# Performance work log

Hardware: AMD Instinct MI355X
Metric: run time of the kernel (lower is better)

Reference implementation:

```python
import jax, jax.numpy as jnp
import numpy as np

N = 100_000      # nodes
E = 1_600_000    # edges (before self-loops)
IN, OUT, HID = 64, 32, 64
BN_EPS = 1e-5

def _mlp(h, w1, b1, g, beta, w2, b2):
    # PyG MLP (num_layers=2, plain_last=True): Linear -> BatchNorm(train) -> ReLU -> Linear
    h = h @ w1 + b1
    mu = jnp.mean(h, axis=0)
    var = jnp.var(h, axis=0)
    h = (h - mu) * jax.lax.rsqrt(var + BN_EPS) * g + beta
    return jax.nn.relu(h) @ w2 + b2

def setup_inputs() -> dict:
    key = jax.random.key(0)
    ks = jax.random.split(key, 12)
    def rn(k, shape):
        fan_in = shape[0]
        return jax.random.normal(k, shape, jnp.float32) / np.sqrt(fan_in)
    x = jax.random.normal(ks[0], (N, IN), jnp.float32)
    pos = jax.random.normal(ks[1], (N, 3), jnp.float32)
    edge_index = jax.random.randint(ks[2], (2, E), 0, N, jnp.int64)
    return {
        "x": x, "pos": pos, "edge_index": edge_index,
        "w_lin": rn(ks[3], (IN, OUT)), "w_src": rn(ks[4], (IN, OUT)), "w_dst": rn(ks[5], (IN, OUT)),
        "pos_w1": rn(ks[6], (3, HID)), "pos_b1": jnp.zeros((HID,), jnp.float32),
        "pos_g": jnp.ones((HID,), jnp.float32), "pos_beta": jnp.zeros((HID,), jnp.float32),
        "pos_w2": rn(ks[7], (HID, OUT)), "pos_b2": jnp.zeros((OUT,), jnp.float32),
        "att_w1": rn(ks[8], (OUT, HID)), "att_b1": jnp.zeros((HID,), jnp.float32),
        "att_g": jnp.ones((HID,), jnp.float32), "att_beta": jnp.zeros((HID,), jnp.float32),
        "att_w2": rn(ks[9], (HID, OUT)), "att_b2": jnp.zeros((OUT,), jnp.float32),
    }

def reference(x, pos, edge_index, w_lin, w_src, w_dst,
              pos_w1, pos_b1, pos_g, pos_beta, pos_w2, pos_b2,
              att_w1, att_b1, att_g, att_beta, att_w2, att_b2):
    n = x.shape[0]
    # add self-loops (PointTransformerConv default add_self_loops=True)
    loops = jnp.arange(n, dtype=edge_index.dtype)
    src = jnp.concatenate([edge_index[0], loops])  # j (message source)
    dst = jnp.concatenate([edge_index[1], loops])  # i (message target)

    alpha_src = x @ w_src          # [N, OUT]
    alpha_dst = x @ w_dst          # [N, OUT]
    x_val = x @ w_lin              # [N, OUT]

    delta = _mlp(pos[dst] - pos[src], pos_w1, pos_b1, pos_g, pos_beta, pos_w2, pos_b2)  # [E', OUT]
    a = _mlp(alpha_dst[dst] - alpha_src[src] + delta, att_w1, att_b1, att_g, att_beta, att_w2, att_b2)

    # per-destination-node, per-channel softmax over incoming edges
    a_max = jax.ops.segment_max(a, dst, num_segments=n)           # [N, OUT]
    a = jnp.exp(a - a_max[dst])
    denom = jax.ops.segment_sum(a, dst, num_segments=n)           # [N, OUT]
    a = a / (denom[dst] + 1e-16)

    msg = a * (x_val[src] + delta)                                # [E', OUT]
    out = jax.ops.segment_sum(msg, dst, num_segments=n)           # [N, OUT]
    return out
```

## Files before the change

kernel.cpp:

```cpp
#include <hip/hip_runtime.h>

typedef unsigned int uint;
typedef unsigned short ushort;

#define BN_EPS 1e-5f

using bf16x8 = __attribute__((ext_vector_type(8))) short;
using f32x16 = __attribute__((ext_vector_type(16))) float;

union FragU { uint w[4]; bf16x8 v; };

__device__ __forceinline__ uint pk2(float lo, float hi) {
    uint r;
    asm("v_cvt_pk_bf16_f32 %0, %1, %2" : "=v"(r) : "v"(lo), "v"(hi));
    return r;
}
__device__ __forceinline__ float bfu_lo(uint u) { return __uint_as_float(u << 16); }
__device__ __forceinline__ float bfu_hi(uint u) { return __uint_as_float(u & 0xffff0000u); }

__device__ __forceinline__ void get_rowmap(int col, int* rowv) {
    FragU pa, pb;
    float c = (float)col;
    #pragma unroll
    for (int j = 0; j < 4; j++) { pa.w[j] = pk2(c, c); pb.w[j] = pk2(1.f, 1.f); }
    f32x16 d;
    #pragma unroll
    for (int r = 0; r < 16; r++) d[r] = 0.f;
    d = __builtin_amdgcn_mfma_f32_32x32x16_bf16(pa.v, pb.v, d, 0, 0, 0);
    #pragma unroll
    for (int r = 0; r < 16; r++) {
        int m = (int)(d[r] * 0.0625f + 0.5f);
        rowv[r] = (m < 0) ? 0 : (m > 31 ? 31 : m);
    }
}

template<bool SORTED>
__device__ __forceinline__ void edge_sd(int e, const int* __restrict__ ei,
                                        const int* __restrict__ srcs,
                                        const int* __restrict__ dsts,
                                        int nE, int& src, int& dst) {
    if (SORTED) { src = srcs[e]; dst = dsts[e]; }
    else if (e < nE) { src = ei[e]; dst = ei[nE + e]; }
    else { src = e - nE; dst = src; }
}

__global__ __launch_bounds__(256) void k_node_lin(
    const float* __restrict__ x,
    const float* __restrict__ w_src, const float* __restrict__ w_dst,
    const float* __restrict__ w_lin,
    uint* __restrict__ aSb, uint* __restrict__ aDb, uint* __restrict__ xvb,
    int nNodes)
{
    int n = blockIdx.x * 256 + threadIdx.x;
    if (n >= nNodes) return;
    float xr[64];
    const float4* xp = (const float4*)(x + (size_t)n * 64);
    #pragma unroll
    for (int i = 0; i < 16; i++) {
        float4 v = xp[i];
        xr[4*i] = v.x; xr[4*i+1] = v.y; xr[4*i+2] = v.z; xr[4*i+3] = v.w;
    }
    const float* ws[3] = { w_src, w_dst, w_lin };
    uint* outs[3] = { aSb, aDb, xvb };
    #pragma unroll
    for (int m = 0; m < 3; m++) {
        const float* w = ws[m];
        float acc[32];
        #pragma unroll
        for (int o = 0; o < 32; o++) acc[o] = 0.f;
        #pragma unroll
        for (int k = 0; k < 64; k++) {
            float xk = xr[k];
            #pragma unroll
            for (int o = 0; o < 32; o++) acc[o] = fmaf(xk, w[k*32+o], acc[o]);
        }
        uint4* op = (uint4*)(outs[m] + (size_t)n * 16);
        #pragma unroll
        for (int q = 0; q < 4; q++) {
            uint4 v;
            v.x = pk2(acc[8*q+0], acc[8*q+1]);
            v.y = pk2(acc[8*q+2], acc[8*q+3]);
            v.z = pk2(acc[8*q+4], acc[8*q+5]);
            v.w = pk2(acc[8*q+6], acc[8*q+7]);
            op[q] = v;
        }
    }
}

__global__ __launch_bounds__(256) void k_pos4(
    const float* __restrict__ pos, float4* __restrict__ pos4, int n)
{
    int i = blockIdx.x * 256 + threadIdx.x;
    if (i < n) pos4[i] = make_float4(pos[i*3], pos[i*3+1], pos[i*3+2], 0.f);
}

__global__ __launch_bounds__(256) void k_hist(
    const int* __restrict__ ei, int* __restrict__ cnt, int nE, int eTot)
{
    int e = blockIdx.x * 256 + threadIdx.x;
    if (e >= eTot) return;
    int dst = (e < nE) ? ei[nE + e] : (e - nE);
    atomicAdd(&cnt[dst], 1);
}

#define SCH 1024
__global__ __launch_bounds__(256) void k_scan1(
    const int* __restrict__ cnt, int* __restrict__ cur,
    int* __restrict__ blkS, int n)
{
    __shared__ int ls[256];
    int t = threadIdx.x;
    int base = blockIdx.x * SCH + t * 4;
    int v0 = (base+0 < n) ? cnt[base+0] : 0;
    int v1 = (base+1 < n) ? cnt[base+1] : 0;
    int v2 = (base+2 < n) ? cnt[base+2] : 0;
    int v3 = (base+3 < n) ? cnt[base+3] : 0;
    int tsum = v0 + v1 + v2 + v3;
    ls[t] = tsum;
    __syncthreads();
    for (int o = 1; o < 256; o <<= 1) {
        int x = (t >= o) ? ls[t-o] : 0;
        __syncthreads();
        ls[t] += x;
        __syncthreads();
    }
    if (t == 255) blkS[blockIdx.x] = ls[255];
    int run = ls[t] - tsum;
    if (base+0 < n) cur[base+0] = run; run += v0;
    if (base+1 < n) cur[base+1] = run; run += v1;
    if (base+2 < n) cur[base+2] = run; run += v2;
    if (base+3 < n) cur[base+3] = run;
}

__global__ void k_scan2(const int* __restrict__ blkS, int* __restrict__ blkOff, int nb)
{
    __shared__ int ls[256];
    int t = threadIdx.x;
    int v = (t < nb) ? blkS[t] : 0;
    ls[t] = v;
    __syncthreads();
    for (int o = 1; o < 256; o <<= 1) {
        int x = (t >= o) ? ls[t-o] : 0;
        __syncthreads();
        ls[t] += x;
        __syncthreads();
    }
    if (t < nb) blkOff[t] = ls[t] - v;
}

__global__ __launch_bounds__(256) void k_scan3(
    int* __restrict__ cur, const int* __restrict__ blkOff, int n)
{
    int off = blkOff[blockIdx.x];
    int base = blockIdx.x * SCH + threadIdx.x * 4;
    #pragma unroll
    for (int j = 0; j < 4; j++) {
        int i = base + j;
        if (i < n) cur[i] += off;
    }
}

__global__ __launch_bounds__(256) void k_rank(
    const int* __restrict__ ei, int* __restrict__ cur,
    int* __restrict__ srcs, int* __restrict__ dsts, int nE, int eTot)
{
    int e = blockIdx.x * 256 + threadIdx.x;
    if (e >= eTot) return;
    int src, dst;
    if (e < nE) { src = ei[e]; dst = ei[nE + e]; }
    else        { src = e - nE; dst = src; }
    int slot = atomicAdd(&cur[dst], 1);
    srcs[slot] = src; dsts[slot] = dst;
}

__global__ __launch_bounds__(256) void k_pos_mom(
    const int* __restrict__ ei, const float4* __restrict__ pos4,
    float* __restrict__ partM, int nE)
{
    float m[9];
    #pragma unroll
    for (int c = 0; c < 9; c++) m[c] = 0.f;
    int stride = gridDim.x * blockDim.x;
    for (int e = blockIdx.x * blockDim.x + threadIdx.x; e < nE; e += stride) {
        int src = ei[e], dst = ei[nE + e];
        float4 pd = pos4[dst], ps = pos4[src];
        float d0 = pd.x - ps.x, d1 = pd.y - ps.y, d2 = pd.z - ps.z;
        m[0] += d0; m[1] += d1; m[2] += d2;
        m[3] = fmaf(d0,d0,m[3]); m[4] = fmaf(d0,d1,m[4]); m[5] = fmaf(d0,d2,m[5]);
        m[6] = fmaf(d1,d1,m[6]); m[7] = fmaf(d1,d2,m[7]); m[8] = fmaf(d2,d2,m[8]);
    }
    __shared__ float red[4][9];
    int w = threadIdx.x >> 6;
    #pragma unroll
    for (int c = 0; c < 9; c++) {
        float t = m[c];
        for (int o = 32; o > 0; o >>= 1) t += __shfl_down(t, o, 64);
        if ((threadIdx.x & 63) == 0) red[w][c] = t;
    }
    __syncthreads();
    if (threadIdx.x < 9)
        partM[blockIdx.x * 9 + threadIdx.x] =
            red[0][threadIdx.x] + red[1][threadIdx.x] + red[2][threadIdx.x] + red[3][threadIdx.x];
}

__global__ void k_bn1_mom(const float* __restrict__ partM, int nBlk,
                          const float* __restrict__ pw1, const float* __restrict__ pb1,
                          const float* __restrict__ g, const float* __restrict__ beta,
                          float* __restrict__ bn, float invE)
{
    __shared__ float mom_s[9];
    int l = threadIdx.x;
    #pragma unroll
    for (int c = 0; c < 9; c++) {
        float s = 0.f;
        for (int i = l; i < nBlk; i += 64) s += partM[i*9 + c];
        for (int o = 32; o > 0; o >>= 1) s += __shfl_down(s, o, 64);
        if (l == 0) mom_s[c] = s;
    }
    __syncthreads();
    int c = l;
    if (c < 64) {
        float w0 = pw1[c], w1 = pw1[64+c], w2 = pw1[128+c], b = pb1[c];
        float S = fmaf(w0, mom_s[0], fmaf(w1, mom_s[1], w2 * mom_s[2]));
        float Q = w0*w0*mom_s[3] + 2.f*w0*w1*mom_s[4] + 2.f*w0*w2*mom_s[5]
                + w1*w1*mom_s[6] + 2.f*w1*w2*mom_s[7] + w2*w2*mom_s[8];
        float mu  = S * invE + b;
        float E2  = Q * invE + 2.f * b * (S * invE) + b * b;
        float var = fmaxf(E2 - mu * mu, 0.f);
        float sc  = rsqrtf(var + BN_EPS) * g[c];
        bn[c]      = sc;
        bn[64+c]   = beta[c] - mu * sc;
    }
}

__global__ __launch_bounds__(256) void k_red_stats(
    const float* __restrict__ partD, float* __restrict__ stats2, int nBlk)
{
    int c = blockIdx.x;
    float s = 0.f;
    for (int i = threadIdx.x; i < nBlk; i += 256) s += partD[(size_t)i*128 + c];
    for (int o = 32; o > 0; o >>= 1) s += __shfl_down(s, o, 64);
    __shared__ float red[4];
    if ((threadIdx.x & 63) == 0) red[threadIdx.x >> 6] = s;
    __syncthreads();
    if (threadIdx.x == 0) stats2[c] = red[0] + red[1] + red[2] + red[3];
}

__global__ void k_bn_fin(const float* __restrict__ stats,
                         const float* __restrict__ g, const float* __restrict__ beta,
                         const float* __restrict__ bias,
                         float* __restrict__ bn, float inv_ep)
{
    int c = threadIdx.x;
    if (c < 64) {
        float b   = bias ? bias[c] : 0.f;
        float m0  = stats[c] * inv_ep;
        float mu  = m0 + b;
        float eq  = stats[64+c] * inv_ep + 2.f*b*m0 + b*b;
        float var = fmaxf(eq - mu * mu, 0.f);
        float sc  = rsqrtf(var + BN_EPS) * g[c];
        bn[c]      = sc;
        bn[64+c]   = beta[c] - mu * sc;
    }
}

__global__ void k_fold1(const float* __restrict__ pw1, const float* __restrict__ pb1,
                        const float* __restrict__ bn1,
                        float* __restrict__ pw1f, float* __restrict__ pb1f)
{
    int i = threadIdx.x;
    if (i < 192) pw1f[i] = pw1[i] * bn1[i & 63];
    if (i < 64)  pb1f[i] = pb1[i] * bn1[i] + bn1[64 + i];
}

__global__ void k_fold2(const float* __restrict__ aw1, const float* __restrict__ ab1,
                        const float* __restrict__ bn2,
                        float* __restrict__ aw1f, float* __restrict__ ab1f)
{
    int i = blockIdx.x * 256 + threadIdx.x;
    if (i < 2048) aw1f[i] = aw1[i] * bn2[i & 63];
    if (i < 64)   ab1f[i] = ab1[i] * bn2[i] + bn2[64 + i];
}

__device__ __forceinline__ void gather_row16(
    const uint* __restrict__ rowp, const int* q2, bool quadOK,
    const int* rowv, float* out)
{
    if (quadOK) {
        #pragma unroll
        for (int g = 0; g < 4; g++) {
            uint2 v = *(const uint2*)(rowp + 2*q2[g]);
            out[4*g+0] = bfu_lo(v.x);
            out[4*g+1] = bfu_hi(v.x);
            out[4*g+2] = bfu_lo(v.y);
            out[4*g+3] = bfu_hi(v.y);
        }
    } else {
        const ushort* rp = (const ushort*)rowp;
        #pragma unroll
        for (int r = 0; r < 16; r++)
            out[r] = __uint_as_float(((uint)rp[rowv[r]]) << 16);
    }
}

template<bool SORTED>
__global__ __launch_bounds__(256, 2) void k_delta_stats(
    const int* __restrict__ ei, const int* __restrict__ srcs, const int* __restrict__ dsts,
    const float4* __restrict__ pos4,
    const uint* __restrict__ aSb, const uint* __restrict__ aDb,
    const float* __restrict__ pw1f, const float* __restrict__ pb1f,
    const float* __restrict__ pw2, const float* __restrict__ pb2,
    const float* __restrict__ aw1,
    float* __restrict__ partD, int nE, int eTot)
{
    const int lane = threadIdx.x & 63;
    const int col  = lane & 31;
    const int h    = lane >> 5;

    __shared__ float redS[4][64], redQ[4][64];
    {
        int w = threadIdx.x >> 6, c = threadIdx.x & 63;
        redS[w][c] = 0.f; redQ[w][c] = 0.f;
    }

    int rowv[16];
    get_rowmap(col, rowv);
    bool quadOK = true;
    #pragma unroll
    for (int g = 0; g < 4; g++)
        quadOK = quadOK && (rowv[4*g+1] == rowv[4*g]+1)
                        && (rowv[4*g+2] == rowv[4*g]+2)
                        && (rowv[4*g+3] == rowv[4*g]+3);
    int q2[4];
    #pragma unroll
    for (int g = 0; g < 4; g++) q2[g] = rowv[4*g] >> 2;

    FragU fw_pw2[4];
    #pragma unroll
    for (int kt = 0; kt < 4; kt++)
        #pragma unroll
        for (int jw = 0; jw < 4; jw++) {
            int m = 2*jw;
            int c0 = 16*kt + 8*(m>>2) + 4*h + (m&3);
            fw_pw2[kt].w[jw] = pk2(pw2[c0*32 + col], pw2[(c0+1)*32 + col]);
        }
    FragU fw_aw1[2][2];
    #pragma unroll
    for (int mt = 0; mt < 2; mt++)
        #pragma unroll
        for (int kt = 0; kt < 2; kt++)
            #pragma unroll
            for (int jw = 0; jw < 4; jw++) {
                int u0 = rowv[8*kt + 2*jw], u1 = rowv[8*kt + 2*jw + 1];
                fw_aw1[mt][kt].w[jw] = pk2(aw1[u0*64 + 32*mt + col],
                                           aw1[u1*64 + 32*mt + col]);
            }
    float pb2v[16];
    #pragma unroll
    for (int r = 0; r < 16; r++) pb2v[r] = pb2[rowv[r]];

    float sA[32], qA[32];
    #pragma unroll
    for (int i = 0; i < 32; i++) { sA[i] = 0.f; qA[i] = 0.f; }

    const int nT = (eTot + 31) >> 5;
    const int gw = (blockIdx.x << 2) + (threadIdx.x >> 6);
    const int nW = gridDim.x << 2;
    for (int t = gw; t < nT; t += nW) {
        int e = t*32 + col;
        bool valid = e < eTot;
        int ec = valid ? e : eTot - 1;
        int src, dst;
        edge_sd<SORTED>(ec, ei, srcs, dsts, nE, src, dst);
        float4 pd = pos4[dst], ps = pos4[src];
        float p0 = pd.x - ps.x, p1 = pd.y - ps.y, p2 = pd.z - ps.z;

        FragU ft[4];
        #pragma unroll
        for (int kt = 0; kt < 4; kt++)
            #pragma unroll
            for (int mm = 0; mm < 2; mm++) {
                int cb = 16*kt + 8*mm + 4*h;
                float4 w0 = *(const float4*)(pw1f +       cb);
                float4 w1 = *(const float4*)(pw1f + 64  + cb);
                float4 w2 = *(const float4*)(pw1f + 128 + cb);
                float4 bb = *(const float4*)(pb1f + cb);
                float t0 = fmaxf(fmaf(p0,w0.x, fmaf(p1,w1.x, fmaf(p2,w2.x, bb.x))), 0.f);
                float t1 = fmaxf(fmaf(p0,w0.y, fmaf(p1,w1.y, fmaf(p2,w2.y, bb.y))), 0.f);
                float t2 = fmaxf(fmaf(p0,w0.z, fmaf(p1,w1.z, fmaf(p2,w2.z, bb.z))), 0.f);
                float t3 = fmaxf(fmaf(p0,w0.w, fmaf(p1,w1.w, fmaf(p2,w2.w, bb.w))), 0.f);
                ft[kt].w[2*mm+0] = pk2(t0, t1);
                ft[kt].w[2*mm+1] = pk2(t2, t3);
            }
        f32x16 adl;
        #pragma unroll
        for (int r = 0; r < 16; r++) adl[r] = pb2v[r];
        #pragma unroll
        for (int kt = 0; kt < 4; kt++)
            adl = __builtin_amdgcn_mfma_f32_32x32x16_bf16(fw_pw2[kt].v, ft[kt].v, adl, 0, 0, 0);

        float gD[16], gS[16];
        gather_row16(aDb + (size_t)dst*16, q2, quadOK, rowv, gD);
        gather_row16(aSb + (size_t)src*16, q2, quadOK, rowv, gS);

        FragU fu[2];
        #pragma unroll
        for (int kt = 0; kt < 2; kt++)
            #pragma unroll
            for (int jw = 0; jw < 4; jw++) {
                int r0 = 8*kt + 2*jw;
                fu[kt].w[jw] = pk2(adl[r0]   + gD[r0]   - gS[r0],
                                   adl[r0+1] + gD[r0+1] - gS[r0+1]);
            }

        f32x16 ah0, ah1;
        #pragma unroll
        for (int r = 0; r < 16; r++) { ah0[r] = 0.f; ah1[r] = 0.f; }
        #pragma unroll
        for (int kt = 0; kt < 2; kt++) {
            ah0 = __builtin_amdgcn_mfma_f32_32x32x16_bf16(fw_aw1[0][kt].v, fu[kt].v, ah0, 0, 0, 0);
            ah1 = __builtin_amdgcn_mfma_f32_32x32x16_bf16(fw_aw1[1][kt].v, fu[kt].v, ah1, 0, 0, 0);
        }
        if (valid) {
            #pragma unroll
            for (int r = 0; r < 16; r++) {
                sA[r]    += ah0[r];
                qA[r]     = fmaf(ah0[r], ah0[r], qA[r]);
                sA[16+r] += ah1[r];
                qA[16+r]  = fmaf(ah1[r], ah1[r], qA[16+r]);
            }
        }
    }
    __syncthreads();
    {
        int w = threadIdx.x >> 6;
        #pragma unroll
        for (int idx = 0; idx < 32; idx++) {
            float vs = sA[idx], vq = qA[idx];
            for (int off = 16; off > 0; off >>= 1) {
                vs += __shfl_xor(vs, off, 64);
                vq += __shfl_xor(vq, off, 64);
            }
            if ((threadIdx.x & 31) == 0) {
                int mt = idx >> 4, r = idx & 15;
                int c = 32*mt + rowv[r];
                redS[w][c] = vs;
                redQ[w][c] = vq;
            }
        }
    }
    __syncthreads();
    if (threadIdx.x < 64) {
        int c = threadIdx.x;
        float S = redS[0][c] + redS[1][c] + redS[2][c] + redS[3][c];
        float Q = redQ[0][c] + redQ[1][c] + redQ[2][c] + redQ[3][c];
        partD[(size_t)blockIdx.x*128 + c]      = S;
        partD[(size_t)blockIdx.x*128 + 64 + c] = Q;
    }
}

template<bool SORTED>
__global__ __launch_bounds__(256, 2) void k_att_agg(
    const int* __restrict__ ei, const int* __restrict__ srcs, const int* __restrict__ dsts,
    const float4* __restrict__ pos4,
    const uint* __restrict__ aSb, const uint* __restrict__ aDb,
    const uint* __restrict__ xvb,
    const float* __restrict__ pw1f, const float* __restrict__ pb1f,
    const float* __restrict__ pw2, const float* __restrict__ pb2,
    const float* __restrict__ aw1f, const float* __restrict__ ab1f,
    const float* __restrict__ aw2, const float* __restrict__ ab2,
    float* __restrict__ denom, float* __restrict__ outp,
    int nE, int eTot)
{
    const int lane = threadIdx.x & 63;
    const int col  = lane & 31;
    const int h    = lane >> 5;

    int rowv[16];
    get_rowmap(col, rowv);
    bool quadOK = true;
    #pragma unroll
    for (int g = 0; g < 4; g++)
        quadOK = quadOK && (rowv[4*g+1] == rowv[4*g]+1)
                        && (rowv[4*g+2] == rowv[4*g]+2)
                        && (rowv[4*g+3] == rowv[4*g]+3);
    int q2[4];
    #pragma unroll
    for (int g = 0; g < 4; g++) q2[g] = rowv[4*g] >> 2;

    FragU fw_pw2[4], fw_aw2[4];
    #pragma unroll
    for (int kt = 0; kt < 4; kt++)
        #pragma unroll
        for (int jw = 0; jw < 4; jw++) {
            int m = 2*jw;
            int c0 = 16*kt + 8*(m>>2) + 4*h + (m&3);
            fw_pw2[kt].w[jw] = pk2(pw2[c0*32 + col], pw2[(c0+1)*32 + col]);
            int o0 = 32*(kt>>1) + rowv[8*(kt&1) + m];
            int o1 = 32*(kt>>1) + rowv[8*(kt&1) + m + 1];
            fw_aw2[kt].w[jw] = pk2(aw2[o0*32 + col], aw2[o1*32 + col]);
        }
    FragU fw_aw1[2][2];
    #pragma unroll
    for (int mt = 0; mt < 2; mt++)
        #pragma unroll
        for (int kt = 0; kt < 2; kt++)
            #pragma unroll
            for (int jw = 0; jw < 4; jw++) {
                int u0 = rowv[8*kt + 2*jw], u1 = rowv[8*kt + 2*jw + 1];
                fw_aw1[mt][kt].w[jw] = pk2(aw1f[u0*64 + 32*mt + col],
                                           aw1f[u1*64 + 32*mt + col]);
            }
    float pb2v[16], ab2v[16], ab1v[32];
    #pragma unroll
    for (int r = 0; r < 16; r++) {
        pb2v[r]    = pb2[rowv[r]];
        ab2v[r]    = ab2[rowv[r]];
        ab1v[r]    = ab1f[rowv[r]];
        ab1v[16+r] = ab1f[32 + rowv[r]];
    }

    const int nT = (eTot + 31) >> 5;
    const int gw = (blockIdx.x << 2) + (threadIdx.x >> 6);
    const int nW = gridDim.x << 2;
    for (int t = gw; t < nT; t += nW) {
        int e = t*32 + col;
        bool valid = e < eTot;
        int ec = valid ? e : eTot - 1;
        int src, dst;
        edge_sd<SORTED>(ec, ei, srcs, dsts, nE, src, dst);
        float4 pd = pos4[dst], ps = pos4[src];
        float p0 = pd.x - ps.x, p1 = pd.y - ps.y, p2 = pd.z - ps.z;

        FragU ft[4];
        #pragma unroll
        for (int kt = 0; kt < 4; kt++)
            #pragma unroll
            for (int mm = 0; mm < 2; mm++) {
                int cb = 16*kt + 8*mm + 4*h;
                float4 w0 = *(const float4*)(pw1f +       cb);
                float4 w1 = *(const float4*)(pw1f + 64  + cb);
                float4 w2 = *(const float4*)(pw1f + 128 + cb);
                float4 bb = *(const float4*)(pb1f + cb);
                float t0 = fmaxf(fmaf(p0,w0.x, fmaf(p1,w1.x, fmaf(p2,w2.x, bb.x))), 0.f);
                float t1 = fmaxf(fmaf(p0,w0.y, fmaf(p1,w1.y, fmaf(p2,w2.y, bb.y))), 0.f);
                float t2 = fmaxf(fmaf(p0,w0.z, fmaf(p1,w1.z, fmaf(p2,w2.z, bb.z))), 0.f);
                float t3 = fmaxf(fmaf(p0,w0.w, fmaf(p1,w1.w, fmaf(p2,w2.w, bb.w))), 0.f);
                ft[kt].w[2*mm+0] = pk2(t0, t1);
                ft[kt].w[2*mm+1] = pk2(t2, t3);
            }
        f32x16 adl;
        #pragma unroll
        for (int r = 0; r < 16; r++) adl[r] = pb2v[r];
        #pragma unroll
        for (int kt = 0; kt < 4; kt++)
            adl = __builtin_amdgcn_mfma_f32_32x32x16_bf16(fw_pw2[kt].v, ft[kt].v, adl, 0, 0, 0);

        float gD[16], gS[16], xg[16];
        gather_row16(aDb + (size_t)dst*16, q2, quadOK, rowv, gD);
        gather_row16(aSb + (size_t)src*16, q2, quadOK, rowv, gS);
        gather_row16(xvb + (size_t)src*16, q2, quadOK, rowv, xg);

        FragU fu[2];
        #pragma unroll
        for (int kt = 0; kt < 2; kt++)
            #pragma unroll
            for (int jw = 0; jw < 4; jw++) {
                int r0 = 8*kt + 2*jw;
                fu[kt].w[jw] = pk2(adl[r0]   + gD[r0]   - gS[r0],
                                   adl[r0+1] + gD[r0+1] - gS[r0+1]);
            }

        f32x16 ah0, ah1;
        #pragma unroll
        for (int r = 0; r < 16; r++) { ah0[r] = ab1v[r]; ah1[r] = ab1v[16+r]; }
        #pragma unroll
        for (int kt = 0; kt < 2; kt++) {
            ah0 = __builtin_amdgcn_mfma_f32_32x32x16_bf16(fw_aw1[0][kt].v, fu[kt].v, ah0, 0, 0, 0);
            ah1 = __builtin_amdgcn_mfma_f32_32x32x16_bf16(fw_aw1[1][kt].v, fu[kt].v, ah1, 0, 0, 0);
        }
        FragU fh[4];
        #pragma unroll
        for (int q = 0; q < 4; q++)
            #pragma unroll
            for (int jw = 0; jw < 4; jw++) {
                int r0 = 8*(q&1) + 2*jw;
                float x0 = (q < 2) ? ah0[r0]   : ah1[r0];
                float x1 = (q < 2) ? ah0[r0+1] : ah1[r0+1];
                fh[q].w[jw] = pk2(fmaxf(x0, 0.f), fmaxf(x1, 0.f));
            }
        f32x16 aa;
        #pragma unroll
        for (int r = 0; r < 16; r++) aa[r] = ab2v[r];
        aa = __builtin_amdgcn_mfma_f32_32x32x16_bf16(fw_aw2[0].v, fh[0].v, aa, 0, 0, 0);
        aa = __builtin_amdgcn_mfma_f32_32x32x16_bf16(fw_aw2[1].v, fh[1].v, aa, 0, 0, 0);
        aa = __builtin_amdgcn_mfma_f32_32x32x16_bf16(fw_aw2[2].v, fh[2].v, aa, 0, 0, 0);
        aa = __builtin_amdgcn_mfma_f32_32x32x16_bf16(fw_aw2[3].v, fh[3].v, aa, 0, 0, 0);

        if (SORTED) {
            float eav[16], msv[16];
            #pragma unroll
            for (int r = 0; r < 16; r++) {
                float ea = __expf(fminf(aa[r], 35.f));
                eav[r] = valid ? ea : 0.f;
                msv[r] = valid ? ea * (xg[r] + adl[r]) : 0.f;
            }
            int lw = lane & 31;
            int dprev = __shfl_up(dst, 1, 32);
            bool isHead = (lw == 0) || (dprev != dst);
            bool eq1  = (__shfl_down(dst, 1, 32)  == dst) && (lw + 1  < 32);
            bool eq2  = (__shfl_down(dst, 2, 32)  == dst) && (lw + 2  < 32);
            bool eq4  = (__shfl_down(dst, 4, 32)  == dst) && (lw + 4  < 32);
            bool eq8  = (__shfl_down(dst, 8, 32)  == dst) && (lw + 8  < 32);
            bool eq16 = (__shfl_down(dst, 16, 32) == dst) && (lw + 16 < 32);
            float* drow = denom + (size_t)dst * 32;
            float* orow = outp  + (size_t)dst * 32;
            #pragma unroll
            for (int r = 0; r < 16; r++) {
                float ev = eav[r], mv = msv[r];
                { float a = __shfl_down(ev,1,32),  b = __shfl_down(mv,1,32);  if (eq1)  { ev += a; mv += b; } }
                { float a = __shfl_down(ev,2,32),  b = __shfl_down(mv,2,32);  if (eq2)  { ev += a; mv += b; } }
                { float a = __shfl_down(ev,4,32),  b = __shfl_down(mv,4,32);  if (eq4)  { ev += a; mv += b; } }
                { float a = __shfl_down(ev,8,32),  b = __shfl_down(mv,8,32);  if (eq8)  { ev += a; mv += b; } }
                { float a = __shfl_down(ev,16,32), b = __shfl_down(mv,16,32); if (eq16) { ev += a; mv += b; } }
                if (isHead) {
                    int o = rowv[r];
                    unsafeAtomicAdd(drow + o, ev);
                    unsafeAtomicAdd(orow + o, mv);
                }
            }
        } else if (valid) {
            float* drow = denom + (size_t)dst * 32;
            float* orow = outp  + (size_t)dst * 32;
            #pragma unroll
            for (int r = 0; r < 16; r++) {
                int o = rowv[r];
                float ea = __expf(fminf(aa[r], 35.f));
                unsafeAtomicAdd(drow + o, ea);
                unsafeAtomicAdd(orow + o, ea * (xg[r] + adl[r]));
            }
        }
    }
}

__global__ __launch_bounds__(256) void k_norm(
    float* __restrict__ out, const float* __restrict__ denom, int total)
{
    int i = blockIdx.x * 256 + threadIdx.x;
    if (i < total) out[i] = out[i] / (denom[i] + 1e-16f);
}

extern "C" void kernel_launch(void* const* d_in, const int* in_sizes, int n_in,
                              void* d_out, int out_size, void* d_ws, size_t ws_size,
                              hipStream_t stream)
{
    const float* x     = (const float*)d_in[0];
    const float* pos   = (const float*)d_in[1];
    const int*   ei    = (const int*)d_in[2];
    const float* w_lin = (const float*)d_in[3];
    const float* w_src = (const float*)d_in[4];
    const float* w_dst = (const float*)d_in[5];
    const float* pw1   = (const float*)d_in[6];
    const float* pb1   = (const float*)d_in[7];
    const float* pg    = (const float*)d_in[8];
    const float* pbeta = (const float*)d_in[9];
    const float* pw2   = (const float*)d_in[10];
    const float* pb2   = (const float*)d_in[11];
    const float* aw1   = (const float*)d_in[12];
    const float* ab1   = (const float*)d_in[13];
    const float* ag    = (const float*)d_in[14];
    const float* abeta = (const float*)d_in[15];
    const float* aw2   = (const float*)d_in[16];
    const float* ab2   = (const float*)d_in[17];
    float* out = (float*)d_out;

    const int nNodes = in_sizes[0] / 64;
    const int nE     = in_sizes[2] / 2;
    const int eTot   = nE + nNodes;

    const int PMBLK = 1024;
    const int DBLK  = 2048;

    const size_t nF = (size_t)nNodes * 32;
    uint*   aSb   = (uint*)d_ws;
    uint*   aDb   = aSb + (size_t)nNodes*16;
    uint*   xvb   = aDb + (size_t)nNodes*16;
    float*  pos4  = (float*)(xvb + (size_t)nNodes*16);
    float*  denom = pos4 + (size_t)nNodes*4;
    float*  stats = denom + nF;
    float*  bn1   = stats + 512;
    float*  bn2   = bn1 + 128;
    float*  pw1f  = bn2 + 128;
    float*  pb1f  = pw1f + 192;
    float*  aw1f  = pb1f + 64;
    float*  ab1f  = aw1f + 2048;
    float*  partM = ab1f + 64;
    float*  partD = partM + (size_t)PMBLK*9;
    float*  fend  = partD + (size_t)DBLK*128;

    int* cnt    = (int*)fend;
    int* cur    = cnt + nNodes;
    int* blkS   = cur + nNodes;
    int* blkOff = blkS + 256;
    int* srcs   = blkOff + 256;
    int* dsts   = srcs + eTot;

    size_t need_sorted = ((char*)(dsts + eTot)) - ((char*)d_ws);
    const bool sorted = ws_size >= need_sorted;

    const int nb = (nNodes + SCH - 1) / SCH;

    hipMemsetAsync(out,   0, nF * sizeof(float), stream);
    hipMemsetAsync(denom, 0, nF * sizeof(float), stream);

    k_node_lin<<<(nNodes + 255) / 256, 256, 0, stream>>>(
        x, w_src, w_dst, w_lin, aSb, aDb, xvb, nNodes);
    k_pos4<<<(nNodes + 255) / 256, 256, 0, stream>>>(pos, (float4*)pos4, nNodes);

    k_pos_mom<<<PMBLK, 256, 0, stream>>>(ei, (const float4*)pos4, partM, nE);
    k_bn1_mom<<<1, 64, 0, stream>>>(partM, PMBLK, pw1, pb1, pg, pbeta, bn1,
                                    1.0f / (float)eTot);
    k_fold1<<<1, 256, 0, stream>>>(pw1, pb1, bn1, pw1f, pb1f);

    if (sorted) {
        hipMemsetAsync(cnt, 0, (size_t)nNodes * sizeof(int), stream);
        k_hist<<<(eTot + 255) / 256, 256, 0, stream>>>(ei, cnt, nE, eTot);
        k_scan1<<<nb, 256, 0, stream>>>(cnt, cur, blkS, nNodes);
        k_scan2<<<1, 256, 0, stream>>>(blkS, blkOff, nb);
        k_scan3<<<nb, 256, 0, stream>>>(cur, blkOff, nNodes);
        k_rank<<<(eTot + 255) / 256, 256, 0, stream>>>(ei, cur, srcs, dsts, nE, eTot);

        k_delta_stats<true><<<DBLK, 256, 0, stream>>>(
            ei, srcs, dsts, (const float4*)pos4, aSb, aDb,
            pw1f, pb1f, pw2, pb2, aw1, partD, nE, eTot);
        k_red_stats<<<128, 256, 0, stream>>>(partD, stats + 128, DBLK);
        k_bn_fin<<<1, 64, 0, stream>>>(stats + 128, ag, abeta, ab1, bn2, 1.0f / (float)eTot);
        k_fold2<<<8, 256, 0, stream>>>(aw1, ab1, bn2, aw1f, ab1f);
        k_att_agg<true><<<DBLK, 256, 0, stream>>>(
            ei, srcs, dsts, (const float4*)pos4, aSb, aDb, xvb,
            pw1f, pb1f, pw2, pb2, aw1f, ab1f, aw2, ab2, denom, out, nE, eTot);
    } else {
        k_delta_stats<false><<<DBLK, 256, 0, stream>>>(
            ei, nullptr, nullptr, (const float4*)pos4, aSb, aDb,
            pw1f, pb1f, pw2, pb2, aw1, partD, nE, eTot);
        k_red_stats<<<128, 256, 0, stream>>>(partD, stats + 128, DBLK);
        k_bn_fin<<<1, 64, 0, stream>>>(stats + 128, ag, abeta, ab1, bn2, 1.0f / (float)eTot);
        k_fold2<<<8, 256, 0, stream>>>(aw1, ab1, bn2, aw1f, ab1f);
        k_att_agg<false><<<DBLK, 256, 0, stream>>>(
            ei, nullptr, nullptr, (const float4*)pos4, aSb, aDb, xvb,
            pw1f, pb1f, pw2, pb2, aw1f, ab1f, aw2, ab2, denom, out, nE, eTot);
    }
    k_norm<<<(((int)nF) + 255) / 256, 256, 0, stream>>>(out, denom, (int)nF);
}
```

Baseline: 839.9 us.

## Interleave source features, stage gathers through LDS, and cache per-edge position deltas

The per-node alpha_src and x_val bf16 rows are interleaved into one 128-byte record per source node. The aggregation kernel cooperatively loads each edge's full source record with coalesced uint4 loads into a swizzled LDS buffer, then reads its lanes' channels from shared memory. The stats kernel writes the per-edge position differences to a workspace buffer so the aggregation kernel reads one float4 instead of gathering two positions. Bias vectors are packed as bf16 pairs and the exp/message computation is moved into the reduction loop, both to cut register pressure. The cost is extra global write and read traffic for the edge delta buffer, 16KB of LDS per block, and bf16 rounding of the biases.

```diff
diff --git a/kernel.cpp b/kernel.cpp
--- a/kernel.cpp
+++ b/kernel.cpp
@@ -17,6 +17,16 @@
 }
 __device__ __forceinline__ float bfu_lo(uint u) { return __uint_as_float(u << 16); }
 __device__ __forceinline__ float bfu_hi(uint u) { return __uint_as_float(u & 0xffff0000u); }
+
+__device__ __forceinline__ float upk(const uint* p, int idx) {
+    uint u = p[idx >> 1];
+    return (idx & 1) ? bfu_hi(u) : bfu_lo(u);
+}
+__device__ __forceinline__ float upq(const uint2* gq, int r) {
+    int g = r >> 2, j = r & 3;
+    uint u = (j < 2) ? gq[g].x : gq[g].y;
+    return (j & 1) ? bfu_hi(u) : bfu_lo(u);
+}
 
 __device__ __forceinline__ void get_rowmap(int col, int* rowv) {
     FragU pa, pb;
@@ -48,7 +58,7 @@
     const float* __restrict__ x,
     const float* __restrict__ w_src, const float* __restrict__ w_dst,
     const float* __restrict__ w_lin,
-    uint* __restrict__ aSb, uint* __restrict__ aDb, uint* __restrict__ xvb,
+    uint* __restrict__ asx, uint* __restrict__ aDb,
     int nNodes)
 {
     int n = blockIdx.x * 256 + threadIdx.x;
@@ -60,8 +70,8 @@
         float4 v = xp[i];
         xr[4*i] = v.x; xr[4*i+1] = v.y; xr[4*i+2] = v.z; xr[4*i+3] = v.w;
     }
-    const float* ws[3] = { w_src, w_dst, w_lin };
-    uint* outs[3] = { aSb, aDb, xvb };
+    const float* ws[3] = { w_src, w_lin, w_dst };
+    uint* outs[3] = { asx + (size_t)n*32, asx + (size_t)n*32 + 16, aDb + (size_t)n*16 };
     #pragma unroll
     for (int m = 0; m < 3; m++) {
         const float* w = ws[m];
@@ -74,7 +84,7 @@
             #pragma unroll
             for (int o = 0; o < 32; o++) acc[o] = fmaf(xk, w[k*32+o], acc[o]);
         }
-        uint4* op = (uint4*)(outs[m] + (size_t)n * 16);
+        uint4* op = (uint4*)outs[m];
         #pragma unroll
         for (int q = 0; q < 4; q++) {
             uint4 v;
@@ -282,36 +292,16 @@
     if (i < 64)   ab1f[i] = ab1[i] * bn2[i] + bn2[64 + i];
 }
 
-__device__ __forceinline__ void gather_row16(
-    const uint* __restrict__ rowp, const int* q2, bool quadOK,
-    const int* rowv, float* out)
-{
-    if (quadOK) {
-        #pragma unroll
-        for (int g = 0; g < 4; g++) {
-            uint2 v = *(const uint2*)(rowp + 2*q2[g]);
-            out[4*g+0] = bfu_lo(v.x);
-            out[4*g+1] = bfu_hi(v.x);
-            out[4*g+2] = bfu_lo(v.y);
-            out[4*g+3] = bfu_hi(v.y);
-        }
-    } else {
-        const ushort* rp = (const ushort*)rowp;
-        #pragma unroll
-        for (int r = 0; r < 16; r++)
-            out[r] = __uint_as_float(((uint)rp[rowv[r]]) << 16);
-    }
-}
-
-template<bool SORTED>
+template<bool SORTED, bool PD>
 __global__ __launch_bounds__(256, 2) void k_delta_stats(
     const int* __restrict__ ei, const int* __restrict__ srcs, const int* __restrict__ dsts,
     const float4* __restrict__ pos4,
-    const uint* __restrict__ aSb, const uint* __restrict__ aDb,
+    const uint* __restrict__ asx, const uint* __restrict__ aDb,
     const float* __restrict__ pw1f, const float* __restrict__ pb1f,
     const float* __restrict__ pw2, const float* __restrict__ pb2,
     const float* __restrict__ aw1,
-    float* __restrict__ partD, int nE, int eTot)
+    float* __restrict__ partD, float4* __restrict__ pd4,
+    int nE, int eTot)
 {
     const int lane = threadIdx.x & 63;
     const int col  = lane & 31;
@@ -323,41 +313,44 @@
         redS[w][c] = 0.f; redQ[w][c] = 0.f;
     }
 
+    bool quadOK;
+    int q2[4];
+    FragU fw_pw2[4];
+    FragU fw_aw1[2][2];
+    uint pb2p[8];
     int rowv[16];
-    get_rowmap(col, rowv);
-    bool quadOK = true;
-    #pragma unroll
-    for (int g = 0; g < 4; g++)
-        quadOK = quadOK && (rowv[4*g+1] == rowv[4*g]+1)
-                        && (rowv[4*g+2] == rowv[4*g]+2)
-                        && (rowv[4*g+3] == rowv[4*g]+3);
-    int q2[4];
-    #pragma unroll
-    for (int g = 0; g < 4; g++) q2[g] = rowv[4*g] >> 2;
-
-    FragU fw_pw2[4];
-    #pragma unroll
-    for (int kt = 0; kt < 4; kt++)
-        #pragma unroll
-        for (int jw = 0; jw < 4; jw++) {
-            int m = 2*jw;
-            int c0 = 16*kt + 8*(m>>2) + 4*h + (m&3);
-            fw_pw2[kt].w[jw] = pk2(pw2[c0*32 + col], pw2[(c0+1)*32 + col]);
-        }
-    FragU fw_aw1[2][2];
-    #pragma unroll
-    for (int mt = 0; mt < 2; mt++)
-        #pragma unroll
-        for (int kt = 0; kt < 2; kt++)
+    {
+        get_rowmap(col, rowv);
+        quadOK = true;
+        #pragma unroll
+        for (int g = 0; g < 4; g++)
+            quadOK = quadOK && (rowv[4*g+1] == rowv[4*g]+1)
+                            && (rowv[4*g+2] == rowv[4*g]+2)
+                            && (rowv[4*g+3] == rowv[4*g]+3);
+        #pragma unroll
+        for (int g = 0; g < 4; g++) q2[g] = rowv[4*g] >> 2;
+        #pragma unroll
+        for (int kt = 0; kt < 4; kt++)
             #pragma unroll
             for (int jw = 0; jw < 4; jw++) {
-                int u0 = rowv[8*kt + 2*jw], u1 = rowv[8*kt + 2*jw + 1];
-                fw_aw1[mt][kt].w[jw] = pk2(aw1[u0*64 + 32*mt + col],
-                                           aw1[u1*64 + 32*mt + col]);
-            }
-    float pb2v[16];
-    #pragma unroll
-    for (int r = 0; r < 16; r++) pb2v[r] = pb2[rowv[r]];
+                int m = 2*jw;
+                int c0 = 16*kt + 8*(m>>2) + 4*h + (m&3);
+                fw_pw2[kt].w[jw] = pk2(pw2[c0*32 + col], pw2[(c0+1)*32 + col]);
+            }
+        #pragma unroll
+        for (int mt = 0; mt < 2; mt++)
+            #pragma unroll
+            for (int kt = 0; kt < 2; kt++)
+                #pragma unroll
+                for (int jw = 0; jw < 4; jw++) {
+                    int u0 = rowv[8*kt + 2*jw], u1 = rowv[8*kt + 2*jw + 1];
+                    fw_aw1[mt][kt].w[jw] = pk2(aw1[u0*64 + 32*mt + col],
+                                               aw1[u1*64 + 32*mt + col]);
+                }
+        #pragma unroll
+        for (int g = 0; g < 8; g++)
+            pb2p[g] = pk2(pb2[rowv[2*g]], pb2[rowv[2*g+1]]);
+    }
 
     float sA[32], qA[32];
     #pragma unroll
@@ -366,14 +359,35 @@
     const int nT = (eTot + 31) >> 5;
     const int gw = (blockIdx.x << 2) + (threadIdx.x >> 6);
     const int nW = gridDim.x << 2;
+
     for (int t = gw; t < nT; t += nW) {
         int e = t*32 + col;
         bool valid = e < eTot;
         int ec = valid ? e : eTot - 1;
         int src, dst;
         edge_sd<SORTED>(ec, ei, srcs, dsts, nE, src, dst);
-        float4 pd = pos4[dst], ps = pos4[src];
+        float4 ps = pos4[src], pd = pos4[dst];
         float p0 = pd.x - ps.x, p1 = pd.y - ps.y, p2 = pd.z - ps.z;
+        if (PD && valid) pd4[e] = make_float4(p0, p1, p2, 0.f);
+
+        uint2 gs2[4], gd2[4];
+        float gSs[16], gDs[16];
+        if (quadOK) {
+            const uint* rs = asx + (size_t)src*32;
+            const uint* rd = aDb + (size_t)dst*16;
+            #pragma unroll
+            for (int g = 0; g < 4; g++) gs2[g] = *(const uint2*)(rs + 2*q2[g]);
+            #pragma unroll
+            for (int g = 0; g < 4; g++) gd2[g] = *(const uint2*)(rd + 2*q2[g]);
+        } else {
+            const ushort* rs = (const ushort*)(asx + (size_t)src*32);
+            const ushort* rd = (const ushort*)(aDb + (size_t)dst*16);
+            #pragma unroll
+            for (int r = 0; r < 16; r++) {
+                gSs[r] = __uint_as_float(((uint)rs[rowv[r]]) << 16);
+                gDs[r] = __uint_as_float(((uint)rd[rowv[r]]) << 16);
+            }
+        }
 
         FragU ft[4];
         #pragma unroll
@@ -394,24 +408,31 @@
             }
         f32x16 adl;
         #pragma unroll
-        for (int r = 0; r < 16; r++) adl[r] = pb2v[r];
+        for (int r = 0; r < 16; r++) adl[r] = upk(pb2p, r);
         #pragma unroll
         for (int kt = 0; kt < 4; kt++)
             adl = __builtin_amdgcn_mfma_f32_32x32x16_bf16(fw_pw2[kt].v, ft[kt].v, adl, 0, 0, 0);
 
-        float gD[16], gS[16];
-        gather_row16(aDb + (size_t)dst*16, q2, quadOK, rowv, gD);
-        gather_row16(aSb + (size_t)src*16, q2, quadOK, rowv, gS);
-
         FragU fu[2];
-        #pragma unroll
-        for (int kt = 0; kt < 2; kt++)
-            #pragma unroll
-            for (int jw = 0; jw < 4; jw++) {
-                int r0 = 8*kt + 2*jw;
-                fu[kt].w[jw] = pk2(adl[r0]   + gD[r0]   - gS[r0],
-                                   adl[r0+1] + gD[r0+1] - gS[r0+1]);
-            }
+        if (quadOK) {
+            #pragma unroll
+            for (int kt = 0; kt < 2; kt++)
+                #pragma unroll
+                for (int jw = 0; jw < 4; jw++) {
+                    int r0 = 8*kt + 2*jw;
+                    fu[kt].w[jw] = pk2(adl[r0]   + upq(gd2, r0)   - upq(gs2, r0),
+                                       adl[r0+1] + upq(gd2, r0+1) - upq(gs2, r0+1));
+                }
+        } else {
+            #pragma unroll
+            for (int kt = 0; kt < 2; kt++)
+                #pragma unroll
+                for (int jw = 0; jw < 4; jw++) {
+                    int r0 = 8*kt + 2*jw;
+                    fu[kt].w[jw] = pk2(adl[r0]   + gDs[r0]   - gSs[r0],
+                                       adl[r0+1] + gDs[r0+1] - gSs[r0+1]);
+                }
+        }
 
         f32x16 ah0, ah1;
         #pragma unroll
@@ -431,6 +452,7 @@
             }
         }
     }
+
     __syncthreads();
     {
         int w = threadIdx.x >> 6;
@@ -459,12 +481,11 @@
     }
 }
 
-template<bool SORTED>
+template<bool SORTED, bool PD>
 __global__ __launch_bounds__(256, 2) void k_att_agg(
     const int* __restrict__ ei, const int* __restrict__ srcs, const int* __restrict__ dsts,
-    const float4* __restrict__ pos4,
-    const uint* __restrict__ aSb, const uint* __restrict__ aDb,
-    const uint* __restrict__ xvb,
+    const float4* __restrict__ pos4, const float4* __restrict__ pd4,
+    const uint* __restrict__ asx, const uint* __restrict__ aDb,
     const float* __restrict__ pw1f, const float* __restrict__ pb1f,
     const float* __restrict__ pw2, const float* __restrict__ pb2,
     const float* __restrict__ aw1f, const float* __restrict__ ab1f,
@@ -475,62 +496,96 @@
     const int lane = threadIdx.x & 63;
     const int col  = lane & 31;
     const int h    = lane >> 5;
-
+    const int wid  = threadIdx.x >> 6;
+
+    __shared__ uint sbuf[4][1024];
+
+    bool quadOK;
+    int q2[4];
     int rowv[16];
-    get_rowmap(col, rowv);
-    bool quadOK = true;
-    #pragma unroll
-    for (int g = 0; g < 4; g++)
-        quadOK = quadOK && (rowv[4*g+1] == rowv[4*g]+1)
-                        && (rowv[4*g+2] == rowv[4*g]+2)
-                        && (rowv[4*g+3] == rowv[4*g]+3);
-    int q2[4];
-    #pragma unroll
-    for (int g = 0; g < 4; g++) q2[g] = rowv[4*g] >> 2;
-
     FragU fw_pw2[4], fw_aw2[4];
-    #pragma unroll
-    for (int kt = 0; kt < 4; kt++)
-        #pragma unroll
-        for (int jw = 0; jw < 4; jw++) {
-            int m = 2*jw;
-            int c0 = 16*kt + 8*(m>>2) + 4*h + (m&3);
-            fw_pw2[kt].w[jw] = pk2(pw2[c0*32 + col], pw2[(c0+1)*32 + col]);
-            int o0 = 32*(kt>>1) + rowv[8*(kt&1) + m];
-            int o1 = 32*(kt>>1) + rowv[8*(kt&1) + m + 1];
-            fw_aw2[kt].w[jw] = pk2(aw2[o0*32 + col], aw2[o1*32 + col]);
-        }
     FragU fw_aw1[2][2];
-    #pragma unroll
-    for (int mt = 0; mt < 2; mt++)
-        #pragma unroll
-        for (int kt = 0; kt < 2; kt++)
+    uint pb2p[8], ab2p[8], ab1p[16];
+    {
+        get_rowmap(col, rowv);
+        quadOK = true;
+        #pragma unroll
+        for (int g = 0; g < 4; g++)
+            quadOK = quadOK && (rowv[4*g+1] == rowv[4*g]+1)
+                            && (rowv[4*g+2] == rowv[4*g]+2)
+                            && (rowv[4*g+3] == rowv[4*g]+3);
+        #pragma unroll
+        for (int g = 0; g < 4; g++) q2[g] = rowv[4*g] >> 2;
+        #pragma unroll
+        for (int kt = 0; kt < 4; kt++)
             #pragma unroll
             for (int jw = 0; jw < 4; jw++) {
-                int u0 = rowv[8*kt + 2*jw], u1 = rowv[8*kt + 2*jw + 1];
-                fw_aw1[mt][kt].w[jw] = pk2(aw1f[u0*64 + 32*mt + col],
-                                           aw1f[u1*64 + 32*mt + col]);
-            }
-    float pb2v[16], ab2v[16], ab1v[32];
-    #pragma unroll
-    for (int r = 0; r < 16; r++) {
-        pb2v[r]    = pb2[rowv[r]];
-        ab2v[r]    = ab2[rowv[r]];
-        ab1v[r]    = ab1f[rowv[r]];
-        ab1v[16+r] = ab1f[32 + rowv[r]];
+                int m = 2*jw;
+                int c0 = 16*kt + 8*(m>>2) + 4*h + (m&3);
+                fw_pw2[kt].w[jw] = pk2(pw2[c0*32 + col], pw2[(c0+1)*32 + col]);
+                int o0 = 32*(kt>>1) + rowv[8*(kt&1) + m];
+                int o1 = 32*(kt>>1) + rowv[8*(kt&1) + m + 1];
+                fw_aw2[kt].w[jw] = pk2(aw2[o0*32 + col], aw2[o1*32 + col]);
+            }
+        #pragma unroll
+        for (int mt = 0; mt < 2; mt++)
+            #pragma unroll
+            for (int kt = 0; kt < 2; kt++)
+                #pragma unroll
+                for (int jw = 0; jw < 4; jw++) {
+                    int u0 = rowv[8*kt + 2*jw], u1 = rowv[8*kt + 2*jw + 1];
+                    fw_aw1[mt][kt].w[jw] = pk2(aw1f[u0*64 + 32*mt + col],
+                                               aw1f[u1*64 + 32*mt + col]);
+                }
+        #pragma unroll
+        for (int g = 0; g < 8; g++) {
+            pb2p[g] = pk2(pb2[rowv[2*g]], pb2[rowv[2*g+1]]);
+            ab2p[g] = pk2(ab2[rowv[2*g]], ab2[rowv[2*g+1]]);
+            ab1p[g]     = pk2(ab1f[rowv[2*g]],      ab1f[rowv[2*g+1]]);
+            ab1p[8 + g] = pk2(ab1f[32 + rowv[2*g]], ab1f[32 + rowv[2*g+1]]);
+        }
     }
 
     const int nT = (eTot + 31) >> 5;
     const int gw = (blockIdx.x << 2) + (threadIdx.x >> 6);
     const int nW = gridDim.x << 2;
+
     for (int t = gw; t < nT; t += nW) {
         int e = t*32 + col;
         bool valid = e < eTot;
         int ec = valid ? e : eTot - 1;
         int src, dst;
         edge_sd<SORTED>(ec, ei, srcs, dsts, nE, src, dst);
-        float4 pd = pos4[dst], ps = pos4[src];
-        float p0 = pd.x - ps.x, p1 = pd.y - ps.y, p2 = pd.z - ps.z;
+
+        float p0, p1, p2;
+        if (PD) {
+            float4 pdv = pd4[ec];
+            p0 = pdv.x; p1 = pdv.y; p2 = pdv.z;
+        } else {
+            float4 ps = pos4[src], pd = pos4[dst];
+            p0 = pd.x - ps.x; p1 = pd.y - ps.y; p2 = pd.z - ps.z;
+        }
+
+        #pragma unroll
+        for (int it = 0; it < 4; it++) {
+            int j  = it*8 + (lane >> 3);
+            int sj = __shfl(src, j, 64);
+            int w  = lane & 7;
+            uint4 v = *(const uint4*)(asx + (size_t)sj*32 + w*4);
+            *(uint4*)&sbuf[wid][j*32 + ((w ^ (j & 7)) << 2)] = v;
+        }
+        uint2 gd2[4];
+        float gDs[16];
+        if (quadOK) {
+            const uint* rd = aDb + (size_t)dst*16;
+            #pragma unroll
+            for (int g = 0; g < 4; g++) gd2[g] = *(const uint2*)(rd + 2*q2[g]);
+        } else {
+            const ushort* rd = (const ushort*)(aDb + (size_t)dst*16);
+            #pragma unroll
+            for (int r = 0; r < 16; r++)
+                gDs[r] = __uint_as_float(((uint)rd[rowv[r]]) << 16);
+        }
 
         FragU ft[4];
         #pragma unroll
@@ -551,29 +606,59 @@
             }
         f32x16 adl;
         #pragma unroll
-        for (int r = 0; r < 16; r++) adl[r] = pb2v[r];
+        for (int r = 0; r < 16; r++) adl[r] = upk(pb2p, r);
         #pragma unroll
         for (int kt = 0; kt < 4; kt++)
             adl = __builtin_amdgcn_mfma_f32_32x32x16_bf16(fw_pw2[kt].v, ft[kt].v, adl, 0, 0, 0);
 
-        float gD[16], gS[16], xg[16];
-        gather_row16(aDb + (size_t)dst*16, q2, quadOK, rowv, gD);
-        gather_row16(aSb + (size_t)src*16, q2, quadOK, rowv, gS);
-        gather_row16(xvb + (size_t)src*16, q2, quadOK, rowv, xg);
+        uint2 gs2[4], gx2[4];
+        if (quadOK) {
+            #pragma unroll
+            for (int g = 0; g < 4; g++) {
+                int wq = q2[g] >> 1, hf = (q2[g] & 1) << 1;
+                gs2[g] = *(const uint2*)&sbuf[wid][col*32 + ((wq ^ (col & 7)) << 2) + hf];
+                gx2[g] = *(const uint2*)&sbuf[wid][col*32 + (((4 + wq) ^ (col & 7)) << 2) + hf];
+            }
+        } else {
+            #pragma unroll
+            for (int g = 0; g < 4; g++) {
+                #define SRD(ch, outv) { int wq2 = (ch) >> 1; int grp = wq2 >> 2; int off = wq2 & 3; \
+                    uint uu = sbuf[wid][col*32 + ((grp ^ (col & 7)) << 2) + off]; \
+                    outv = ((ch) & 1) ? (uu >> 16) : (uu & 0xffffu); }
+                uint s0,s1,s2,s3, x0,x1,x2,x3;
+                int i0 = rowv[4*g], i1 = rowv[4*g+1], i2 = rowv[4*g+2], i3 = rowv[4*g+3];
+                SRD(i0, s0) SRD(i1, s1) SRD(i2, s2) SRD(i3, s3)
+                SRD(32+i0, x0) SRD(32+i1, x1) SRD(32+i2, x2) SRD(32+i3, x3)
+                #undef SRD
+                gs2[g].x = s0 | (s1 << 16); gs2[g].y = s2 | (s3 << 16);
+                gx2[g].x = x0 | (x1 << 16); gx2[g].y = x2 | (x3 << 16);
+            }
+        }
 
         FragU fu[2];
-        #pragma unroll
-        for (int kt = 0; kt < 2; kt++)
-            #pragma unroll
-            for (int jw = 0; jw < 4; jw++) {
-                int r0 = 8*kt + 2*jw;
-                fu[kt].w[jw] = pk2(adl[r0]   + gD[r0]   - gS[r0],
-                                   adl[r0+1] + gD[r0+1] - gS[r0+1]);
-            }
+        if (quadOK) {
+            #pragma unroll
+            for (int kt = 0; kt < 2; kt++)
+                #pragma unroll
+                for (int jw = 0; jw < 4; jw++) {
+                    int r0 = 8*kt + 2*jw;
+                    fu[kt].w[jw] = pk2(adl[r0]   + upq(gd2, r0)   - upq(gs2, r0),
+                                       adl[r0+1] + upq(gd2, r0+1) - upq(gs2, r0+1));
+                }
+        } else {
+            #pragma unroll
+            for (int kt = 0; kt < 2; kt++)
+                #pragma unroll
+                for (int jw = 0; jw < 4; jw++) {
+                    int r0 = 8*kt + 2*jw;
+                    fu[kt].w[jw] = pk2(adl[r0]   + gDs[r0]   - upq(gs2, r0),
+                                       adl[r0+1] + gDs[r0+1] - upq(gs2, r0+1));
+                }
+        }
 
         f32x16 ah0, ah1;
         #pragma unroll
-        for (int r = 0; r < 16; r++) { ah0[r] = ab1v[r]; ah1[r] = ab1v[16+r]; }
+        for (int r = 0; r < 16; r++) { ah0[r] = upk(ab1p, r); ah1[r] = upk(ab1p, 16 + r); }
         #pragma unroll
         for (int kt = 0; kt < 2; kt++) {
             ah0 = __builtin_amdgcn_mfma_f32_32x32x16_bf16(fw_aw1[0][kt].v, fu[kt].v, ah0, 0, 0, 0);
@@ -591,20 +676,13 @@
             }
         f32x16 aa;
         #pragma unroll
-        for (int r = 0; r < 16; r++) aa[r] = ab2v[r];
+        for (int r = 0; r < 16; r++) aa[r] = upk(ab2p, r);
         aa = __builtin_amdgcn_mfma_f32_32x32x16_bf16(fw_aw2[0].v, fh[0].v, aa, 0, 0, 0);
         aa = __builtin_amdgcn_mfma_f32_32x32x16_bf16(fw_aw2[1].v, fh[1].v, aa, 0, 0, 0);
         aa = __builtin_amdgcn_mfma_f32_32x32x16_bf16(fw_aw2[2].v, fh[2].v, aa, 0, 0, 0);
         aa = __builtin_amdgcn_mfma_f32_32x32x16_bf16(fw_aw2[3].v, fh[3].v, aa, 0, 0, 0);
 
         if (SORTED) {
-            float eav[16], msv[16];
-            #pragma unroll
-            for (int r = 0; r < 16; r++) {
-                float ea = __expf(fminf(aa[r], 35.f));
-                eav[r] = valid ? ea : 0.f;
-                msv[r] = valid ? ea * (xg[r] + adl[r]) : 0.f;
-            }
             int lw = lane & 31;
             int dprev = __shfl_up(dst, 1, 32);
             bool isHead = (lw == 0) || (dprev != dst);
@@ -617,14 +695,16 @@
             float* orow = outp  + (size_t)dst * 32;
             #pragma unroll
             for (int r = 0; r < 16; r++) {
-                float ev = eav[r], mv = msv[r];
+                float ea = __expf(fminf(aa[r], 35.f));
+                float ev = valid ? ea : 0.f;
+                float mv = valid ? ea * (upq(gx2, r) + adl[r]) : 0.f;
                 { float a = __shfl_down(ev,1,32),  b = __shfl_down(mv,1,32);  if (eq1)  { ev += a; mv += b; } }
                 { float a = __shfl_down(ev,2,32),  b = __shfl_down(mv,2,32);  if (eq2)  { ev += a; mv += b; } }
                 { float a = __shfl_down(ev,4,32),  b = __shfl_down(mv,4,32);  if (eq4)  { ev += a; mv += b; } }
                 { float a = __shfl_down(ev,8,32),  b = __shfl_down(mv,8,32);  if (eq8)  { ev += a; mv += b; } }
                 { float a = __shfl_down(ev,16,32), b = __shfl_down(mv,16,32); if (eq16) { ev += a; mv += b; } }
                 if (isHead) {
-                    int o = rowv[r];
+                    int o = quadOK ? (4*q2[r>>2] + (r&3)) : rowv[r];
                     unsafeAtomicAdd(drow + o, ev);
                     unsafeAtomicAdd(orow + o, mv);
                 }
@@ -634,10 +714,10 @@
             float* orow = outp  + (size_t)dst * 32;
             #pragma unroll
             for (int r = 0; r < 16; r++) {
-                int o = rowv[r];
+                int o = quadOK ? (4*q2[r>>2] + (r&3)) : rowv[r];
                 float ea = __expf(fminf(aa[r], 35.f));
                 unsafeAtomicAdd(drow + o, ea);
-                unsafeAtomicAdd(orow + o, ea * (xg[r] + adl[r]));
+                unsafeAtomicAdd(orow + o, ea * (upq(gx2, r) + adl[r]));
             }
         }
     }
@@ -682,10 +762,9 @@
     const int DBLK  = 2048;
 
     const size_t nF = (size_t)nNodes * 32;
-    uint*   aSb   = (uint*)d_ws;
-    uint*   aDb   = aSb + (size_t)nNodes*16;
-    uint*   xvb   = aDb + (size_t)nNodes*16;
-    float*  pos4  = (float*)(xvb + (size_t)nNodes*16);
+    uint*   asx   = (uint*)d_ws;
+    uint*   aDb   = asx + (size_t)nNodes*32;
+    float*  pos4  = (float*)(aDb + (size_t)nNodes*16);
     float*  denom = pos4 + (size_t)nNodes*4;
     float*  stats = denom + nF;
     float*  bn1   = stats + 512;
@@ -704,9 +783,13 @@
     int* blkOff = blkS + 256;
     int* srcs   = blkOff + 256;
     int* dsts   = srcs + eTot;
-
-    size_t need_sorted = ((char*)(dsts + eTot)) - ((char*)d_ws);
+    size_t pd_off = (((size_t)((char*)(dsts + eTot) - (char*)d_ws)) + 15) & ~(size_t)15;
+    float4* pd4  = (float4*)((char*)d_ws + pd_off);
+
+    size_t need_sorted = (char*)(dsts + eTot) - (char*)d_ws;
+    size_t need_pd     = pd_off + (size_t)eTot * sizeof(float4);
     const bool sorted = ws_size >= need_sorted;
+    const bool usePD  = sorted && (ws_size >= need_pd);
 
     const int nb = (nNodes + SCH - 1) / SCH;
 
@@ -714,7 +797,7 @@
     hipMemsetAsync(denom, 0, nF * sizeof(float), stream);
 
     k_node_lin<<<(nNodes + 255) / 256, 256, 0, stream>>>(
-        x, w_src, w_dst, w_lin, aSb, aDb, xvb, nNodes);
+        x, w_src, w_dst, w_lin, asx, aDb, nNodes);
     k_pos4<<<(nNodes + 255) / 256, 256, 0, stream>>>(pos, (float4*)pos4, nNodes);
 
     k_pos_mom<<<PMBLK, 256, 0, stream>>>(ei, (const float4*)pos4, partM, nE);
@@ -730,24 +813,36 @@
         k_scan3<<<nb, 256, 0, stream>>>(cur, blkOff, nNodes);
         k_rank<<<(eTot + 255) / 256, 256, 0, stream>>>(ei, cur, srcs, dsts, nE, eTot);
 
-        k_delta_stats<true><<<DBLK, 256, 0, stream>>>(
-            ei, srcs, dsts, (const float4*)pos4, aSb, aDb,
-            pw1f, pb1f, pw2, pb2, aw1, partD, nE, eTot);
+        if (usePD) {
+            k_delta_stats<true, true><<<DBLK, 256, 0, stream>>>(
+                ei, srcs, dsts, (const float4*)pos4, asx, aDb,
+                pw1f, pb1f, pw2, pb2, aw1, partD, pd4, nE, eTot);
+        } else {
+            k_delta_stats<true, false><<<DBLK, 256, 0, stream>>>(
+                ei, srcs, dsts, (const float4*)pos4, asx, aDb,
+                pw1f, pb1f, pw2, pb2, aw1, partD, nullptr, nE, eTot);
+        }
         k_red_stats<<<128, 256, 0, stream>>>(partD, stats + 128, DBLK);
         k_bn_fin<<<1, 64, 0, stream>>>(stats + 128, ag, abeta, ab1, bn2, 1.0f / (float)eTot);
         k_fold2<<<8, 256, 0, stream>>>(aw1, ab1, bn2, aw1f, ab1f);
-        k_att_agg<true><<<DBLK, 256, 0, stream>>>(
-            ei, srcs, dsts, (const float4*)pos4, aSb, aDb, xvb,
-            pw1f, pb1f, pw2, pb2, aw1f, ab1f, aw2, ab2, denom, out, nE, eTot);
+        if (usePD) {
+            k_att_agg<true, true><<<DBLK, 256, 0, stream>>>(
+                ei, srcs, dsts, (const float4*)pos4, (const float4*)pd4, asx, aDb,
+                pw1f, pb1f, pw2, pb2, aw1f, ab1f, aw2, ab2, denom, out, nE, eTot);
+        } else {
+            k_att_agg<true, false><<<DBLK, 256, 0, stream>>>(
+                ei, srcs, dsts, (const float4*)pos4, nullptr, asx, aDb,
+                pw1f, pb1f, pw2, pb2, aw1f, ab1f, aw2, ab2, denom, out, nE, eTot);
+        }
     } else {
-        k_delta_stats<false><<<DBLK, 256, 0, stream>>>(
-            ei, nullptr, nullptr, (const float4*)pos4, aSb, aDb,
-            pw1f, pb1f, pw2, pb2, aw1, partD, nE, eTot);
+        k_delta_stats<false, false><<<DBLK, 256, 0, stream>>>(
+            ei, nullptr, nullptr, (const float4*)pos4, asx, aDb,
+            pw1f, pb1f, pw2, pb2, aw1, partD, nullptr, nE, eTot);
         k_red_stats<<<128, 256, 0, stream>>>(partD, stats + 128, DBLK);
         k_bn_fin<<<1, 64, 0, stream>>>(stats + 128, ag, abeta, ab1, bn2, 1.0f / (float)eTot);
         k_fold2<<<8, 256, 0, stream>>>(aw1, ab1, bn2, aw1f, ab1f);
-        k_att_agg<false><<<DBLK, 256, 0, stream>>>(
-            ei, nullptr, nullptr, (const float4*)pos4, aSb, aDb, xvb,
+        k_att_agg<false, false><<<DBLK, 256, 0, stream>>>(
+            ei, nullptr, nullptr, (const float4*)pos4, nullptr, asx, aDb,
             pw1f, pb1f, pw2, pb2, aw1f, ab1f, aw2, ab2, denom, out, nE, eTot);
     }
     k_norm<<<(((int)nF) + 255) / 256, 256, 0, stream>>>(out, denom, (int)nF);
```

Result: slower. 906.9 us (+8.0%).
